# Kernel optimization log

Hardware: AMD Instinct MI355X
Metric: run time of the kernel (lower is better)

The kernel has to match this reference:

```python
import jax, jax.numpy as jnp
import numpy as np

HEADS = 4
DIM_HEAD = 32
SCALE = DIM_HEAD ** -0.5

# Energy conventions (Hopfield / Lagrangian formulation):
#  Neuron(x): g = activation(x); e = sum(x*g) - L(x)
#  Synapse(g, x): e = -sum(g*x)
#  identity Lagrangian: L(x) = 0.5*sum(x^2), g = x  => Conv2d block energy = -0.5*sum(x^2)
#  softmax Lagrangian: L(x) = sum(logsumexp(x, -1)), g = softmax(x, -1)

def setup_inputs() -> dict:
    key = jax.random.key(0)
    ks = jax.random.split(key, 5)
    b, c, h, w = 8, 256, 48, 48
    hidden = HEADS * DIM_HEAD  # 128
    return {
        "x": jax.random.normal(ks[0], (b, c, h, w), jnp.float32),
        "w_qkv": jax.random.normal(ks[1], (hidden * 3, c), jnp.float32) * 0.02,
        "b_qkv": jax.random.normal(ks[2], (hidden * 3,), jnp.float32) * 0.02,
        "w_out": jax.random.normal(ks[3], (c, hidden), jnp.float32) * 0.02,
        "b_out": jax.random.normal(ks[4], (c,), jnp.float32) * 0.02,
    }

def reference(x, w_qkv, b_qkv, w_out, b_out):
    b, c, h, w = x.shape
    # 1x1 conv == channel matmul
    qkv = jnp.einsum('oc,bcxy->boxy', w_qkv, x) + b_qkv[None, :, None, None]
    e_qkv = -0.5 * jnp.sum(qkv * qkv)  # identity-Lagrangian neuron + synapse energy
    q, k, v = jnp.split(qkv, 3, axis=1)
    # 'b (h c) x y -> b h c (x y)'
    def heads(t):
        return t.reshape(b, HEADS, DIM_HEAD, h * w)
    q, k, v = heads(q), heads(k), heads(v)
    q = q * SCALE
    sim = jnp.einsum('bhdi,bhdj->bhij', q, k)  # [b, heads, hw, hw]
    sim = sim - jax.lax.stop_gradient(jnp.max(sim, axis=-1, keepdims=True))
    attn = jax.nn.softmax(sim, axis=-1)
    # softmax-Lagrangian neuron energy: sum(sim*attn) - sum(logsumexp(sim, -1))
    e_attn = jnp.sum(sim * attn) - jnp.sum(jax.nn.logsumexp(sim, axis=-1))
    out = jnp.einsum('bhij,bhdj->bhid', attn, v)  # [b, heads, hw, dim_head]
    # 'b h (x y) d -> b (h d) x y'
    out = out.transpose(0, 1, 3, 2).reshape(b, HEADS * DIM_HEAD, h, w)
    out = jnp.einsum('oc,bcxy->boxy', w_out, out) + b_out[None, :, None, None]
    e_out = -0.5 * jnp.sum(out * out)
    return out, e_attn + e_out + e_qkv
```

## Files before the change

### kernel.cpp

```cpp
#include <hip/hip_runtime.h>
#include <hip/hip_bf16.h>

#define HW 2304
#define NB 8
#define NC 256
#define HID 128
#define DH 32
#define NH 4
#define SCALE 0.17677669529663687f
#define LOG2E 1.4426950408889634f
#define LN2   0.6931471805599453f

#define NSPLIT 4
#define OSZ ((size_t)NB * HW * HID)

using bf16x8 = __attribute__((ext_vector_type(8))) short;
using f32x4  = __attribute__((ext_vector_type(4))) float;

__device__ __forceinline__ short f2bf(float f) {
    unsigned u = __float_as_uint(f);
    u += 0x7FFF + ((u >> 16) & 1);
    return (short)(u >> 16);
}
__device__ __forceinline__ float bf2f(short s) {
    return __uint_as_float(((unsigned)(unsigned short)s) << 16);
}
__device__ __forceinline__ unsigned pk2bf(float a, float b) {
    union { __hip_bfloat162 h; unsigned u; } cv;
    cv.h = __float22bfloat162_rn(float2{a, b});
    return cv.u;
}
__device__ __forceinline__ void gld16(const void* g, void* l) {
    __builtin_amdgcn_global_load_lds(
        (const __attribute__((address_space(1))) unsigned*)g,
        (__attribute__((address_space(3))) unsigned*)l, 16, 0, 0);
}
#define SB() __builtin_amdgcn_sched_barrier(0)

__global__ __launch_bounds__(256)
void prep(const float* __restrict__ x, const float* __restrict__ wq,
          const float* __restrict__ wo, short* __restrict__ Xt,
          short* __restrict__ Wq, short* __restrict__ Wo, float* __restrict__ wsz)
{
    if (blockIdx.z == 8) {
        const int bid = blockIdx.x + 72 * blockIdx.y;
        if (bid == 0 && threadIdx.x == 0) { wsz[0] = 0.f; ((int*)wsz)[1] = 0; }
        const int i = bid * 256 + threadIdx.x;
        if (i < 384 * 256) Wq[i] = f2bf(wq[i]);
        if (i < 256 * 128) Wo[i] = f2bf(wo[i]);
        return;
    }
    __shared__ float T[32][33];
    const int b = blockIdx.z, c0 = blockIdx.y * 32, s0 = blockIdx.x * 32;
    const int ts = threadIdx.x & 31, tc = threadIdx.x >> 5;
    #pragma unroll
    for (int cc = tc; cc < 32; cc += 8)
        T[cc][ts] = x[((size_t)b * NC + c0 + cc) * HW + s0 + ts];
    __syncthreads();
    const int tcc = threadIdx.x & 31, tss = threadIdx.x >> 5;
    #pragma unroll
    for (int ss = tss; ss < 32; ss += 8)
        Xt[((size_t)b * HW + s0 + ss) * NC + c0 + tcc] = f2bf(T[tcc][ss]);
}

__global__ __launch_bounds__(256, 2)
void conv_qkv(const short* __restrict__ A, const short* __restrict__ Bt,
              const float* __restrict__ bias,
              short* __restrict__ Qb, short* __restrict__ Kb,
              short* __restrict__ Vb, float* __restrict__ E)
{
    constexpr int KD = NC;
    constexpr int NI = KD / 32;
    const int b  = blockIdx.z;
    const int bm = blockIdx.y * 64;
    const int bn = blockIdx.x * 128;
    const int t  = threadIdx.x;
    const int w  = t >> 6, lane = t & 63;
    const int n16 = lane & 15, quad = lane >> 4;

    __shared__ __align__(16) char csm[4 * 12288];
    __shared__ float red[4];

    const int rL = lane >> 2, cswz = (lane & 3) ^ (rL & 3);
    const char* agl = (const char*)(A  + (size_t)(bm + rL) * KD + cswz * 8);
    const char* bgl = (const char*)(Bt + ((size_t)b * HW + bn + rL) * KD + cswz * 8);

    auto issue = [&](int kc, int pbuf) {
        char* base = csm + pbuf * 12288;
        if (w == 0) {
            gld16(agl + (size_t)(0 * 16 * KD + kc) * 2, base + 0 * 1024);
            gld16(agl + (size_t)(1 * 16 * KD + kc) * 2, base + 1 * 1024);
            gld16(bgl + (size_t)(0 * 16 * KD + kc) * 2, base + 4096 + 0 * 1024);
        } else if (w == 1) {
            gld16(agl + (size_t)(2 * 16 * KD + kc) * 2, base + 2 * 1024);
            gld16(agl + (size_t)(3 * 16 * KD + kc) * 2, base + 3 * 1024);
            gld16(bgl + (size_t)(1 * 16 * KD + kc) * 2, base + 4096 + 1 * 1024);
        } else if (w == 2) {
            gld16(bgl + (size_t)(2 * 16 * KD + kc) * 2, base + 4096 + 2 * 1024);
            gld16(bgl + (size_t)(3 * 16 * KD + kc) * 2, base + 4096 + 3 * 1024);
            gld16(bgl + (size_t)(4 * 16 * KD + kc) * 2, base + 4096 + 4 * 1024);
        } else {
            gld16(bgl + (size_t)(5 * 16 * KD + kc) * 2, base + 4096 + 5 * 1024);
            gld16(bgl + (size_t)(6 * 16 * KD + kc) * 2, base + 4096 + 6 * 1024);
            gld16(bgl + (size_t)(7 * 16 * KD + kc) * 2, base + 4096 + 7 * 1024);
        }
    };

    f32x4 acc[4][2] = {};
    const int rsw = (quad ^ (n16 & 3)) * 16;

    issue(0, 0); SB();
    issue(32, 1); SB();
    for (int ki = 0; ki < NI; ++ki) {
        if (ki + 2 < NI) {
            issue((ki + 2) * 32, (ki + 2) & 3);
            asm volatile("s_waitcnt vmcnt(6)" ::: "memory");
        } else if (ki + 2 == NI) {
            asm volatile("s_waitcnt vmcnt(3)" ::: "memory");
        } else {
            asm volatile("s_waitcnt vmcnt(0)" ::: "memory");
        }
        __builtin_amdgcn_s_barrier();
        SB();

        const char* Ap = csm + (ki & 3) * 12288;
        const char* Bp = Ap + 4096;
        bf16x8 am[4], bq[2];
        #pragma unroll
        for (int tm = 0; tm < 4; ++tm)
            am[tm] = *(const bf16x8*)(Ap + tm * 1024 + n16 * 64 + rsw);
        #pragma unroll
        for (int j = 0; j < 2; ++j)
            bq[j] = *(const bf16x8*)(Bp + (w * 2 + j) * 1024 + n16 * 64 + rsw);
        #pragma unroll
        for (int tm = 0; tm < 4; ++tm)
            #pragma unroll
            for (int j = 0; j < 2; ++j)
                acc[tm][j] = __builtin_amdgcn_mfma_f32_16x16x32_bf16(am[tm], bq[j], acc[tm][j], 0, 0, 0);
    }

    float e = 0.f;
    #pragma unroll
    for (int tm = 0; tm < 4; ++tm) {
        const int o0 = bm + tm * 16 + quad * 4;
        const float4 bb = *(const float4*)(bias + o0);
        #pragma unroll
        for (int j = 0; j < 2; ++j) {
            const int s = bn + (w * 2 + j) * 16 + n16;
            float v[4] = {acc[tm][j][0] + bb.x, acc[tm][j][1] + bb.y,
                          acc[tm][j][2] + bb.z, acc[tm][j][3] + bb.w};
            e -= 0.5f * (v[0]*v[0] + v[1]*v[1] + v[2]*v[2] + v[3]*v[3]);
            if (o0 < HID) {
                const int h = o0 >> 5, dh0 = o0 & 31;
                const float qs = SCALE * LOG2E;
                short4 pk = {f2bf(v[0]*qs), f2bf(v[1]*qs),
                             f2bf(v[2]*qs), f2bf(v[3]*qs)};
                *(short4*)(Qb + ((size_t)(b * NH + h) * HW + s) * DH + dh0) = pk;
            } else if (o0 < 2 * HID) {
                const int c = o0 - HID, h = c >> 5, dh0 = c & 31;
                const int g = s & 31;
                const int sp = (s & ~31) | ((g & 4) << 2) | ((g >> 3) << 2) | (g & 3);
                short4 pk = {f2bf(v[0]), f2bf(v[1]), f2bf(v[2]), f2bf(v[3])};
                *(short4*)(Kb + ((size_t)(b * NH + h) * HW + sp) * DH + dh0) = pk;
            } else {
                const int c = o0 - 2 * HID, h = c >> 5, dh0 = c & 31;
                #pragma unroll
                for (int r = 0; r < 4; ++r)
                    Vb[((size_t)(b * NH + h) * DH + dh0 + r) * HW + s] = f2bf(v[r]);
            }
        }
    }

    #pragma unroll
    for (int off = 32; off > 0; off >>= 1) e += __shfl_down(e, off);
    if (lane == 0) red[w] = e;
    __syncthreads();
    if (t == 0) atomicAdd(E, red[0] + red[1] + red[2] + red[3]);
}

__global__ __launch_bounds__(256)
void flashsplit(const short* __restrict__ Qb, const short* __restrict__ Kb,
                const short* __restrict__ Vb, short* __restrict__ Oh,
                float* __restrict__ lsP, float* __restrict__ tsP)
{
    __shared__ __align__(16) char smem[4 * 8192];

    constexpr int ITERS = HW / (NSPLIT * 64);
    const int bh   = blockIdx.y;
    const int kh   = blockIdx.z;
    const int w    = threadIdx.x >> 6;
    const int lane = threadIdx.x & 63;
    const int n16  = lane & 15, quad = lane >> 4;
    const int qb   = blockIdx.x * 128 + w * 32;

    bf16x8 aq[2];
    #pragma unroll
    for (int qg = 0; qg < 2; ++qg)
        aq[qg] = *(const bf16x8*)(Qb + ((size_t)bh * HW + qb + qg * 16 + n16) * DH + quad * 8);
    SB();

    const int rL = lane >> 2, cL = (lane & 3) ^ (rL & 3);
    const char* gbase; size_t gstep;
    if (w < 2) {
        gbase = (const char*)(Kb + (size_t)bh * HW * DH) + ((w & 1) * 16 + rL) * 64 + cL * 16;
        gstep = 2048;
    } else {
        gbase = (const char*)(Vb + (size_t)bh * DH * HW)
              + (size_t)((w & 1) * 16 + rL) * (HW * 2) + cL * 16;
        gstep = 64;
    }
    gbase += (size_t)kh * (2 * ITERS) * gstep;

    gld16(gbase,             smem + 0 * 8192 + 0    + w * 1024);
    gld16(gbase + gstep,     smem + 0 * 8192 + 4096 + w * 1024);
    SB();
    gld16(gbase + 2 * gstep, smem + 1 * 8192 + 0    + w * 1024);
    gld16(gbase + 3 * gstep, smem + 1 * 8192 + 4096 + w * 1024);
    SB();
    const char* gnext = gbase + 4 * gstep;

    f32x4 acc[2][2] = {};
    float ls[2] = {}, ts[2] = {};
    const int swz = (quad ^ (n16 & 3)) * 8;

    for (int it = 0; it < ITERS; ++it) {
        if (it + 2 < ITERS) {
            char* wb = smem + ((it + 2) & 3) * 8192;
            gld16(gnext,         wb + 0    + w * 1024);
            gld16(gnext + gstep, wb + 4096 + w * 1024);
            gnext += 2 * gstep;
            asm volatile("s_waitcnt vmcnt(4)" ::: "memory");
        } else if (it + 2 == ITERS) {
            asm volatile("s_waitcnt vmcnt(2)" ::: "memory");
        } else {
            asm volatile("s_waitcnt vmcnt(0)" ::: "memory");
        }
        __builtin_amdgcn_s_barrier();
        SB();

        const char* buf = smem + (it & 3) * 8192;
        #pragma unroll
        for (int ca = 0; ca < 2; ++ca) {
            const short* kb = (const short*)(buf + ca * 4096);

            const bf16x8 bk0 = *(const bf16x8*)(kb + n16 * 32 + swz);
            const bf16x8 bk1 = *(const bf16x8*)(kb + 512  + n16 * 32 + swz);
            const bf16x8 bv0 = *(const bf16x8*)(kb + 1024 + n16 * 32 + swz);
            const bf16x8 bv1 = *(const bf16x8*)(kb + 1536 + n16 * 32 + swz);

            #pragma unroll
            for (int qg = 0; qg < 2; ++qg) {
                f32x4 z = {};
                const f32x4 s0 = __builtin_amdgcn_mfma_f32_16x16x32_bf16(bk0, aq[qg], z, 0, 0, 0);
                const f32x4 s1 = __builtin_amdgcn_mfma_f32_16x16x32_bf16(bk1, aq[qg], z, 0, 0, 0);
                float e0[4], e1[4];
                #pragma unroll
                for (int r = 0; r < 4; ++r) {
                    e0[r] = __builtin_amdgcn_exp2f(s0[r]);
                    e1[r] = __builtin_amdgcn_exp2f(s1[r]);
                }
                ls[qg] += (e0[0] + e0[1]) + (e0[2] + e0[3])
                        + (e1[0] + e1[1]) + (e1[2] + e1[3]);
                ts[qg] += (e0[0]*s0[0] + e0[1]*s0[1]) + (e0[2]*s0[2] + e0[3]*s0[3])
                        + (e1[0]*s1[0] + e1[1]*s1[1]) + (e1[2]*s1[2] + e1[3]*s1[3]);
                union { bf16x8 v; unsigned u[4]; } pa;
                pa.u[0] = pk2bf(e0[0], e0[1]);
                pa.u[1] = pk2bf(e0[2], e0[3]);
                pa.u[2] = pk2bf(e1[0], e1[1]);
                pa.u[3] = pk2bf(e1[2], e1[3]);
                acc[qg][0] = __builtin_amdgcn_mfma_f32_16x16x32_bf16(bv0, pa.v, acc[qg][0], 0, 0, 0);
                acc[qg][1] = __builtin_amdgcn_mfma_f32_16x16x32_bf16(bv1, pa.v, acc[qg][1], 0, 0, 0);
            }
        }
    }

    #pragma unroll
    for (int qg = 0; qg < 2; ++qg) {
        ls[qg] += __shfl_xor(ls[qg], 16);
        ls[qg] += __shfl_xor(ls[qg], 32);
        ts[qg] += __shfl_xor(ts[qg], 16);
        ts[qg] += __shfl_xor(ts[qg], 32);
    }

    const int bb = bh >> 2, h = bh & 3;
    short* dst = Oh + (size_t)kh * OSZ;
    #pragma unroll
    for (int qg = 0; qg < 2; ++qg) {
        const int q = qb + qg * 16 + n16;
        const float L = ls[qg];
        const float invl = 1.f / L;
        short* ap = dst + ((size_t)bb * HW + q) * HID + h * 32;
        short4 pk0 = {f2bf(acc[qg][0][0] * invl), f2bf(acc[qg][0][1] * invl),
                      f2bf(acc[qg][0][2] * invl), f2bf(acc[qg][0][3] * invl)};
        short4 pk1 = {f2bf(acc[qg][1][0] * invl), f2bf(acc[qg][1][1] * invl),
                      f2bf(acc[qg][1][2] * invl), f2bf(acc[qg][1][3] * invl)};
        *(short4*)(ap + quad * 4)      = pk0;
        *(short4*)(ap + 16 + quad * 4) = pk1;
        if (quad == 0) {
            const size_t li = (size_t)(kh * 32 + bh) * HW + q;
            lsP[li] = L;
            tsP[li] = ts[qg];
        }
    }
}

__global__ __launch_bounds__(256, 2)
void conv_out(const short* __restrict__ A, const short* __restrict__ Oh,
              const float* __restrict__ lsP, const float* __restrict__ tsP,
              const float* __restrict__ bias, float* __restrict__ out0,
              float* __restrict__ E, int* __restrict__ ticket, int nblocks,
              float* __restrict__ edst)
{
    constexpr int KD = HID;
    constexpr int NI = KD / 32;
    const int b  = blockIdx.z;
    const int bm = blockIdx.y * 64;
    const int bn = blockIdx.x * 128;
    const int t  = threadIdx.x;
    const int w  = t >> 6, lane = t & 63;
    const int n16 = lane & 15, quad = lane >> 4;

    __shared__ __align__(16) char csm[24576];
    __shared__ float red[4];

    const int rL = lane >> 2, cswz = (lane & 3) ^ (rL & 3);
    const char* agl = (const char*)(A + (size_t)(bm + rL) * KD + cswz * 8);

    auto issueA = [&](int kc, int pbuf) {
        char* base = csm + pbuf * 12288;
        if (w == 0) {
            gld16(agl + (size_t)(0 * 16 * KD + kc) * 2, base + 0 * 1024);
            gld16(agl + (size_t)(1 * 16 * KD + kc) * 2, base + 1 * 1024);
        } else if (w == 1) {
            gld16(agl + (size_t)(2 * 16 * KD + kc) * 2, base + 2 * 1024);
            gld16(agl + (size_t)(3 * 16 * KD + kc) * 2, base + 3 * 1024);
        }
    };

    auto loadB = [&](int ki, bf16x8 pk[2]) {
        const int kc = ki * 32;
        const int bh = b * NH + ki;
        #pragma unroll
        for (int d = 0; d < 2; ++d) {
            const int blk = w * 2 + d;
            const int q = bn + blk * 16 + rL;
            float Ls[NSPLIT], sum = 0.f;
            #pragma unroll
            for (int kh = 0; kh < NSPLIT; ++kh) {
                Ls[kh] = lsP[(size_t)(kh * 32 + bh) * HW + q];
                sum += Ls[kh];
            }
            const float inv = 1.f / sum;
            float vv[8] = {};
            #pragma unroll
            for (int kh = 0; kh < NSPLIT; ++kh) {
                const float wk = Ls[kh] * inv;
                const bf16x8 o = *(const bf16x8*)(Oh + (size_t)kh * OSZ
                                    + ((size_t)b * HW + q) * HID + kc + cswz * 8);
                #pragma unroll
                for (int j = 0; j < 8; ++j) vv[j] += wk * bf2f(o[j]);
            }
            union { bf16x8 v; unsigned u[4]; } c;
            #pragma unroll
            for (int i = 0; i < 4; ++i) c.u[i] = pk2bf(vv[2*i], vv[2*i+1]);
            pk[d] = c.v;
        }
    };
    auto writeB = [&](const bf16x8 pk[2], int pbuf) {
        char* base = csm + pbuf * 12288 + 4096;
        #pragma unroll
        for (int d = 0; d < 2; ++d) {
            const int blk = w * 2 + d;
            *(bf16x8*)(base + blk * 1024 + rL * 64 + (lane & 3) * 16) = pk[d];
        }
    };

    f32x4 acc[4][2] = {};
    const int rsw = (quad ^ (n16 & 3)) * 16;

    bf16x8 bpk[2];
    loadB(0, bpk);
    issueA(0, 0);
    writeB(bpk, 0);
    for (int ki = 0; ki < NI; ++ki) {
        const int p = ki & 1;
        __syncthreads();
        if (ki + 1 < NI) { loadB(ki + 1, bpk); issueA((ki + 1) * 32, p ^ 1); }

        const char* Ap = csm + p * 12288;
        const char* Bp = Ap + 4096;
        bf16x8 am[4], bq[2];
        #pragma unroll
        for (int tm = 0; tm < 4; ++tm)
            am[tm] = *(const bf16x8*)(Ap + tm * 1024 + n16 * 64 + rsw);
        #pragma unroll
        for (int j = 0; j < 2; ++j)
            bq[j] = *(const bf16x8*)(Bp + (w * 2 + j) * 1024 + n16 * 64 + rsw);
        #pragma unroll
        for (int tm = 0; tm < 4; ++tm)
            #pragma unroll
            for (int j = 0; j < 2; ++j)
                acc[tm][j] = __builtin_amdgcn_mfma_f32_16x16x32_bf16(am[tm], bq[j], acc[tm][j], 0, 0, 0);

        if (ki + 1 < NI) writeB(bpk, p ^ 1);
    }

    float e = 0.f;
    #pragma unroll
    for (int tm = 0; tm < 4; ++tm) {
        const int o0 = bm + tm * 16 + quad * 4;
        const float4 bb = *(const float4*)(bias + o0);
        #pragma unroll
        for (int j = 0; j < 2; ++j) {
            const int s = bn + (w * 2 + j) * 16 + n16;
            float v[4] = {acc[tm][j][0] + bb.x, acc[tm][j][1] + bb.y,
                          acc[tm][j][2] + bb.z, acc[tm][j][3] + bb.w};
            e -= 0.5f * (v[0]*v[0] + v[1]*v[1] + v[2]*v[2] + v[3]*v[3]);
            #pragma unroll
            for (int r = 0; r < 4; ++r)
                out0[((size_t)b * NC + o0 + r) * HW + s] = v[r];
        }
    }

    if (blockIdx.y == 0) {
        const int q = bn + (t & 127);
        #pragma unroll
        for (int jj = 0; jj < 2; ++jj) {
            const int h = (t >> 7) * 2 + jj;
            const int bh = b * NH + h;
            float L = 0.f, T = 0.f;
            #pragma unroll
            for (int kh = 0; kh < NSPLIT; ++kh) {
                L += lsP[(size_t)(kh * 32 + bh) * HW + q];
                T += tsP[(size_t)(kh * 32 + bh) * HW + q];
            }
            e += (LN2 * T) / L - __logf(L);
        }
    }

    #pragma unroll
    for (int off = 32; off > 0; off >>= 1) e += __shfl_down(e, off);
    if (lane == 0) red[w] = e;
    __syncthreads();
    if (t == 0) {
        atomicAdd(E, red[0] + red[1] + red[2] + red[3]);
        __threadfence();
        const int prev = atomicAdd(ticket, 1);
        if (prev == nblocks - 1) {
            __threadfence();
            edst[0] = atomicAdd(E, 0.f);
        }
    }
}

extern "C" void kernel_launch(void* const* d_in, const int* in_sizes, int n_in,
                              void* d_out, int out_size, void* d_ws, size_t ws_size,
                              hipStream_t stream) {
    const float* x     = (const float*)d_in[0];
    const float* w_qkv = (const float*)d_in[1];
    const float* b_qkv = (const float*)d_in[2];
    const float* w_out = (const float*)d_in[3];
    const float* b_out = (const float*)d_in[4];
    float* out = (float*)d_out;

    float* wsf    = (float*)d_ws;
    float* E      = wsf;
    int*   ticket = (int*)d_ws + 1;
    short* Xt   = (short*)(wsf + 16);
    short* Wq   = Xt + (size_t)NB * HW * NC;
    short* Wo   = Wq + 384 * 256;
    short* Qb   = Wo + 256 * 128;
    short* Kb   = Qb + (size_t)NB * NH * HW * DH;
    short* Vb   = Kb + (size_t)NB * NH * HW * DH;
    short* Oh   = Vb + (size_t)NB * NH * HW * DH;
    float* lsP  = (float*)(Oh + NSPLIT * OSZ);
    float* tsP  = lsP + NSPLIT * 32 * HW;

    prep<<<dim3(HW / 32, NC / 32, NB + 1), 256, 0, stream>>>(
        x, w_qkv, w_out, Xt, Wq, Wo, wsf);
    conv_qkv<<<dim3(18, 6, NB), 256, 0, stream>>>(
        Wq, Xt, b_qkv, Qb, Kb, Vb, E);
    flashsplit<<<dim3(HW / 128, NB * NH, NSPLIT), 256, 0, stream>>>(
        Qb, Kb, Vb, Oh, lsP, tsP);
    conv_out<<<dim3(18, 4, NB), 256, 0, stream>>>(
        Wo, Oh, lsP, tsP, b_out, out, E, ticket, 18 * 4 * NB,
        out + (size_t)NB * NC * HW);
}
```

Baseline: 197.1 us.

## Compute softmax row sums and energy terms via MFMA with transposed K

Replaces the per-element VALU accumulation of exp sums and exp*score sums with MFMA work. Row sums come from a matmul against a vector of ones, and the sum of p*s is rewritten as q·(P K^T), using a transposed copy of K written by the QKV conv. The flash kernel now stages K, V and K^T in a two-buffer pipeline that waits on all loads each iteration, in place of the four-buffer pipeline. This offloads VALU work onto the matrix cores but adds three extra MFMAs per step, an extra K^T write and read, shallower prefetch, and lower precision because p is rounded to bf16 before summing.

```diff
diff --git a/kernel.cpp b/kernel.cpp
--- a/kernel.cpp
+++ b/kernel.cpp
@@ -2,6 +2,7 @@
 #include <hip/hip_bf16.h>
 
 #define HW 2304
+#define HW2 4608
 #define NB 8
 #define NC 256
 #define HID 128
@@ -67,7 +68,8 @@
 void conv_qkv(const short* __restrict__ A, const short* __restrict__ Bt,
               const float* __restrict__ bias,
               short* __restrict__ Qb, short* __restrict__ Kb,
-              short* __restrict__ Vb, float* __restrict__ E)
+              short* __restrict__ Kt, short* __restrict__ Vb,
+              float* __restrict__ E)
 {
     constexpr int KD = NC;
     constexpr int NI = KD / 32;
@@ -162,6 +164,9 @@
                 const int sp = (s & ~31) | ((g & 4) << 2) | ((g >> 3) << 2) | (g & 3);
                 short4 pk = {f2bf(v[0]), f2bf(v[1]), f2bf(v[2]), f2bf(v[3])};
                 *(short4*)(Kb + ((size_t)(b * NH + h) * HW + sp) * DH + dh0) = pk;
+                #pragma unroll
+                for (int r = 0; r < 4; ++r)
+                    Kt[((size_t)(b * NH + h) * DH + dh0 + r) * HW + s] = f2bf(v[r]);
             } else {
                 const int c = o0 - 2 * HID, h = c >> 5, dh0 = c & 31;
                 #pragma unroll
@@ -180,10 +185,11 @@
 
 __global__ __launch_bounds__(256)
 void flashsplit(const short* __restrict__ Qb, const short* __restrict__ Kb,
-                const short* __restrict__ Vb, short* __restrict__ Oh,
-                float* __restrict__ lsP, float* __restrict__ tsP)
+                const short* __restrict__ Kt, const short* __restrict__ Vb,
+                short* __restrict__ Oh, float* __restrict__ lsP,
+                float* __restrict__ tsP)
 {
-    __shared__ __align__(16) char smem[4 * 8192];
+    __shared__ __align__(16) char smem[2 * 12288];
 
     constexpr int ITERS = HW / (NSPLIT * 64);
     const int bh   = blockIdx.y;
@@ -192,6 +198,7 @@
     const int lane = threadIdx.x & 63;
     const int n16  = lane & 15, quad = lane >> 4;
     const int qb   = blockIdx.x * 128 + w * 32;
+    const int key0 = kh * ITERS * 64;
 
     bf16x8 aq[2];
     #pragma unroll
@@ -200,53 +207,58 @@
     SB();
 
     const int rL = lane >> 2, cL = (lane & 3) ^ (rL & 3);
-    const char* gbase; size_t gstep;
-    if (w < 2) {
-        gbase = (const char*)(Kb + (size_t)bh * HW * DH) + ((w & 1) * 16 + rL) * 64 + cL * 16;
-        gstep = 2048;
-    } else {
-        gbase = (const char*)(Vb + (size_t)bh * DH * HW)
-              + (size_t)((w & 1) * 16 + rL) * (HW * 2) + cL * 16;
-        gstep = 64;
-    }
-    gbase += (size_t)kh * (2 * ITERS) * gstep;
-
-    gld16(gbase,             smem + 0 * 8192 + 0    + w * 1024);
-    gld16(gbase + gstep,     smem + 0 * 8192 + 4096 + w * 1024);
+    const char* Kglb  = (const char*)(Kb + (size_t)bh * HW * DH);
+    const char* Vglb  = (const char*)(Vb + (size_t)bh * DH * HW);
+    const char* Ktglb = (const char*)(Kt + (size_t)bh * DH * HW);
+    const int pca  = w & 1;
+    const int ktca = w >> 1;
+    const int ktu  = w & 1;
+
+    auto stage = [&](int it, int pbuf) {
+        char* buf = smem + pbuf * 12288;
+        const int k64 = key0 + it * 64;
+        if (w < 2) {
+            const char* kg = Kglb + (size_t)(k64 + pca * 32 + rL) * 64 + cL * 16;
+            gld16(kg,        buf + pca * 6144 + 0);
+            gld16(kg + 1024, buf + pca * 6144 + 1024);
+        } else {
+            const char* vg = Vglb + (size_t)rL * HW2 + (size_t)(k64 + pca * 32) * 2 + cL * 16;
+            gld16(vg,             buf + pca * 6144 + 2048);
+            gld16(vg + 16 * HW2,  buf + pca * 6144 + 3072);
+        }
+        const char* kt = Ktglb + (size_t)(ktu * 16 + rL) * HW2
+                       + (size_t)(k64 + ktca * 32) * 2 + cL * 16;
+        gld16(kt, buf + ktca * 6144 + 4096 + ktu * 1024);
+    };
+
+    stage(0, 0);
     SB();
-    gld16(gbase + 2 * gstep, smem + 1 * 8192 + 0    + w * 1024);
-    gld16(gbase + 3 * gstep, smem + 1 * 8192 + 4096 + w * 1024);
-    SB();
-    const char* gnext = gbase + 4 * gstep;
 
     f32x4 acc[2][2] = {};
-    float ls[2] = {}, ts[2] = {};
+    f32x4 lsacc[2] = {};
+    f32x4 tsacc[2][2] = {};
     const int swz = (quad ^ (n16 & 3)) * 8;
+    const bf16x8 ones = {0x3F80, 0x3F80, 0x3F80, 0x3F80,
+                         0x3F80, 0x3F80, 0x3F80, 0x3F80};
 
     for (int it = 0; it < ITERS; ++it) {
-        if (it + 2 < ITERS) {
-            char* wb = smem + ((it + 2) & 3) * 8192;
-            gld16(gnext,         wb + 0    + w * 1024);
-            gld16(gnext + gstep, wb + 4096 + w * 1024);
-            gnext += 2 * gstep;
-            asm volatile("s_waitcnt vmcnt(4)" ::: "memory");
-        } else if (it + 2 == ITERS) {
-            asm volatile("s_waitcnt vmcnt(2)" ::: "memory");
-        } else {
-            asm volatile("s_waitcnt vmcnt(0)" ::: "memory");
-        }
+        const int p = it & 1;
+        asm volatile("s_waitcnt vmcnt(0)" ::: "memory");
         __builtin_amdgcn_s_barrier();
         SB();
-
-        const char* buf = smem + (it & 3) * 8192;
+        if (it + 1 < ITERS) stage(it + 1, p ^ 1);
+
+        const char* buf = smem + p * 12288;
         #pragma unroll
         for (int ca = 0; ca < 2; ++ca) {
-            const short* kb = (const short*)(buf + ca * 4096);
-
-            const bf16x8 bk0 = *(const bf16x8*)(kb + n16 * 32 + swz);
-            const bf16x8 bk1 = *(const bf16x8*)(kb + 512  + n16 * 32 + swz);
-            const bf16x8 bv0 = *(const bf16x8*)(kb + 1024 + n16 * 32 + swz);
-            const bf16x8 bv1 = *(const bf16x8*)(kb + 1536 + n16 * 32 + swz);
+            const short* cb = (const short*)(buf + ca * 6144);
+
+            const bf16x8 bk0  = *(const bf16x8*)(cb +        n16 * 32 + swz);
+            const bf16x8 bk1  = *(const bf16x8*)(cb + 512  + n16 * 32 + swz);
+            const bf16x8 bv0  = *(const bf16x8*)(cb + 1024 + n16 * 32 + swz);
+            const bf16x8 bv1  = *(const bf16x8*)(cb + 1536 + n16 * 32 + swz);
+            const bf16x8 bkt0 = *(const bf16x8*)(cb + 2048 + n16 * 32 + swz);
+            const bf16x8 bkt1 = *(const bf16x8*)(cb + 2560 + n16 * 32 + swz);
 
             #pragma unroll
             for (int qg = 0; qg < 2; ++qg) {
@@ -259,27 +271,18 @@
                     e0[r] = __builtin_amdgcn_exp2f(s0[r]);
                     e1[r] = __builtin_amdgcn_exp2f(s1[r]);
                 }
-                ls[qg] += (e0[0] + e0[1]) + (e0[2] + e0[3])
-                        + (e1[0] + e1[1]) + (e1[2] + e1[3]);
-                ts[qg] += (e0[0]*s0[0] + e0[1]*s0[1]) + (e0[2]*s0[2] + e0[3]*s0[3])
-                        + (e1[0]*s1[0] + e1[1]*s1[1]) + (e1[2]*s1[2] + e1[3]*s1[3]);
                 union { bf16x8 v; unsigned u[4]; } pa;
                 pa.u[0] = pk2bf(e0[0], e0[1]);
                 pa.u[1] = pk2bf(e0[2], e0[3]);
                 pa.u[2] = pk2bf(e1[0], e1[1]);
                 pa.u[3] = pk2bf(e1[2], e1[3]);
-                acc[qg][0] = __builtin_amdgcn_mfma_f32_16x16x32_bf16(bv0, pa.v, acc[qg][0], 0, 0, 0);
-                acc[qg][1] = __builtin_amdgcn_mfma_f32_16x16x32_bf16(bv1, pa.v, acc[qg][1], 0, 0, 0);
+                acc[qg][0]   = __builtin_amdgcn_mfma_f32_16x16x32_bf16(bv0,  pa.v, acc[qg][0], 0, 0, 0);
+                acc[qg][1]   = __builtin_amdgcn_mfma_f32_16x16x32_bf16(bv1,  pa.v, acc[qg][1], 0, 0, 0);
+                lsacc[qg]    = __builtin_amdgcn_mfma_f32_16x16x32_bf16(ones, pa.v, lsacc[qg], 0, 0, 0);
+                tsacc[qg][0] = __builtin_amdgcn_mfma_f32_16x16x32_bf16(bkt0, pa.v, tsacc[qg][0], 0, 0, 0);
+                tsacc[qg][1] = __builtin_amdgcn_mfma_f32_16x16x32_bf16(bkt1, pa.v, tsacc[qg][1], 0, 0, 0);
             }
         }
-    }
-
-    #pragma unroll
-    for (int qg = 0; qg < 2; ++qg) {
-        ls[qg] += __shfl_xor(ls[qg], 16);
-        ls[qg] += __shfl_xor(ls[qg], 32);
-        ts[qg] += __shfl_xor(ts[qg], 16);
-        ts[qg] += __shfl_xor(ts[qg], 32);
     }
 
     const int bb = bh >> 2, h = bh & 3;
@@ -287,7 +290,16 @@
     #pragma unroll
     for (int qg = 0; qg < 2; ++qg) {
         const int q = qb + qg * 16 + n16;
-        const float L = ls[qg];
+        const float L = lsacc[qg][0];
+        const short4 qa = *(const short4*)(Qb + ((size_t)bh * HW + q) * DH + quad * 4);
+        const short4 qc = *(const short4*)(Qb + ((size_t)bh * HW + q) * DH + 16 + quad * 4);
+        float ts = bf2f(qa.x) * tsacc[qg][0][0] + bf2f(qa.y) * tsacc[qg][0][1]
+                 + bf2f(qa.z) * tsacc[qg][0][2] + bf2f(qa.w) * tsacc[qg][0][3]
+                 + bf2f(qc.x) * tsacc[qg][1][0] + bf2f(qc.y) * tsacc[qg][1][1]
+                 + bf2f(qc.z) * tsacc[qg][1][2] + bf2f(qc.w) * tsacc[qg][1][3];
+        ts += __shfl_xor(ts, 16);
+        ts += __shfl_xor(ts, 32);
+
         const float invl = 1.f / L;
         short* ap = dst + ((size_t)bb * HW + q) * HID + h * 32;
         short4 pk0 = {f2bf(acc[qg][0][0] * invl), f2bf(acc[qg][0][1] * invl),
@@ -299,7 +311,7 @@
         if (quad == 0) {
             const size_t li = (size_t)(kh * 32 + bh) * HW + q;
             lsP[li] = L;
-            tsP[li] = ts[qg];
+            tsP[li] = ts;
         }
     }
 }
@@ -471,7 +483,8 @@
     short* Wo   = Wq + 384 * 256;
     short* Qb   = Wo + 256 * 128;
     short* Kb   = Qb + (size_t)NB * NH * HW * DH;
-    short* Vb   = Kb + (size_t)NB * NH * HW * DH;
+    short* Ktb  = Kb + (size_t)NB * NH * HW * DH;
+    short* Vb   = Ktb + (size_t)NB * NH * HW * DH;
     short* Oh   = Vb + (size_t)NB * NH * HW * DH;
     float* lsP  = (float*)(Oh + NSPLIT * OSZ);
     float* tsP  = lsP + NSPLIT * 32 * HW;
@@ -479,9 +492,9 @@
     prep<<<dim3(HW / 32, NC / 32, NB + 1), 256, 0, stream>>>(
         x, w_qkv, w_out, Xt, Wq, Wo, wsf);
     conv_qkv<<<dim3(18, 6, NB), 256, 0, stream>>>(
-        Wq, Xt, b_qkv, Qb, Kb, Vb, E);
+        Wq, Xt, b_qkv, Qb, Kb, Ktb, Vb, E);
     flashsplit<<<dim3(HW / 128, NB * NH, NSPLIT), 256, 0, stream>>>(
-        Qb, Kb, Vb, Oh, lsP, tsP);
+        Qb, Kb, Ktb, Vb, Oh, lsP, tsP);
     conv_out<<<dim3(18, 4, NB), 256, 0, stream>>>(
         Wo, Oh, lsP, tsP, b_out, out, E, ticket, 18 * 4 * NB,
         out + (size_t)NB * NC * HW);
```

Result: no change. 196.1 us (-0.5%).
